# Kernel tuning notes

Measured on AMD Instinct MI355X. Metric: run time of the kernel, lower is better.

The kernel has to match this reference:

```python
import jax, jax.numpy as jnp
import numpy as np

N = 4096          # number of bodies
DIM = 2           # 2D physics (Parallax robot soccer)
K_BROAD = 4 * N   # broad phase keeps first 4N AABB overlaps (per source)
K_EXACT = N       # exact phase keeps first N true penetrations (per source)


def setup_inputs() -> dict:
    key = jax.random.key(0)
    k1, k2 = jax.random.split(key)
    # disk bodies scattered in a ~160x160 arena -> dense enough for many hits
    pos = jax.random.normal(k1, (N, DIM), dtype=jnp.float32) * 40.0
    radius = jax.random.uniform(k2, (N,), dtype=jnp.float32, minval=0.5, maxval=1.5)
    return {"pos": pos, "radius": radius}


def _forward(pos, radius):
    n = pos.shape[0]
    # ---- broad phase: sphere AABB = pos +- radius; two boxes overlap iff
    # |p_i - p_j| <= r_i + r_j on every axis. Full O(N^2) scan (as in source),
    # compact the first K_BROAD hits in row-major (i*n + j) order.
    d = jnp.abs(pos[:, None, :] - pos[None, :, :])            # [N,N,DIM]
    rsum = radius[:, None] + radius[None, :]                  # [N,N]
    overlap = jnp.all(d <= rsum[..., None], axis=-1)          # [N,N] bool
    overlap = overlap & ~jnp.eye(n, dtype=bool)               # skip self-pairs
    flat = overlap.reshape(-1)                                # [N*N]
    rank = jnp.cumsum(flat.astype(jnp.int32)) - 1             # slot of each hit
    valid = flat & (rank < K_BROAD)
    slot = jnp.where(valid, rank, K_BROAD)                    # K_BROAD -> dropped
    ii = jnp.repeat(jnp.arange(n, dtype=jnp.int32), n)
    jj = jnp.tile(jnp.arange(n, dtype=jnp.int32), n)
    bi = jnp.full((K_BROAD,), -1, jnp.int32).at[slot].set(ii, mode='drop')
    bj = jnp.full((K_BROAD,), -1, jnp.int32).at[slot].set(jj, mode='drop')
    # ---- exact phase: sphere-sphere penetration test on broad pairs,
    # keep first K_EXACT real penetrations (gather-compute-compact).
    gi = jnp.clip(bi, 0, n - 1)
    gj = jnp.clip(bj, 0, n - 1)
    dv = pos[gi] - pos[gj]                                    # [K_BROAD,DIM]
    dist = jnp.sqrt(jnp.sum(dv * dv, axis=-1) + 1e-12)
    pen_depth = radius[gi] + radius[gj] - dist                # >0 means overlap
    hit = (bi >= 0) & (pen_depth > 0)
    erank = jnp.cumsum(hit.astype(jnp.int32)) - 1
    evalid = hit & (erank < K_EXACT)
    eslot = jnp.where(evalid, erank, K_EXACT)                 # K_EXACT -> dropped
    pen_vec = dv * (pen_depth / dist)[:, None]                # penetration vector
    ei = jnp.full((K_EXACT,), -1, jnp.int32).at[eslot].set(bi, mode='drop')
    ej = jnp.full((K_EXACT,), -1, jnp.int32).at[eslot].set(bj, mode='drop')
    ev = jnp.zeros((K_EXACT, pos.shape[-1]), pos.dtype).at[eslot].set(pen_vec, mode='drop')
    # ---- resolve: each body of the pair is pushed half the penetration apart,
    si = jnp.where(ei >= 0, ei, n)                            # n -> dropped
    sj = jnp.where(ej >= 0, ej, n)
    new_i = pos[jnp.clip(ei, 0, n - 1)] + 0.5 * ev
    new_j = pos[jnp.clip(ej, 0, n - 1)] - 0.5 * ev
    out = pos.at[si].set(new_i, mode='drop')
    out = out.at[sj].set(new_j, mode='drop')
    return out


def reference(pos, radius):
    return _forward(pos, radius)
```

## Files before the change

### kernel.cpp

```cpp
#include <hip/hip_runtime.h>

#define NB 4096
#define KBROAD (4 * NB)
#define KEXACT NB
typedef unsigned long long u64;

__global__ __launch_bounds__(256) void count_kernel(
    const float2* __restrict__ pos, const float* __restrict__ rad,
    int* __restrict__ row_counts, u64* __restrict__ masks,
    int* __restrict__ last_key) {
  int gid = blockIdx.x * blockDim.x + threadIdx.x;
  if (gid < NB) last_key[gid] = -1;
  int wave = gid >> 6;
  int lane = gid & 63;
  int r0 = wave * 2;
  float2 p0 = pos[r0], p1 = pos[r0 + 1];
  float ra0 = rad[r0], ra1 = rad[r0 + 1];
  u64 mw0 = 0, mw1 = 0;
  int c0 = 0, c1 = 0;
  for (int c = 0; c < 64; ++c) {
    int j = c * 64 + lane;
    float2 pj = pos[j];
    float rj = rad[j];
    float rs0 = ra0 + rj, rs1 = ra1 + rj;
    bool h0 = (j != r0) && (fabsf(p0.x - pj.x) <= rs0) && (fabsf(p0.y - pj.y) <= rs0);
    bool h1 = (j != r0 + 1) && (fabsf(p1.x - pj.x) <= rs1) && (fabsf(p1.y - pj.y) <= rs1);
    u64 m0 = __ballot(h0);
    u64 m1 = __ballot(h1);
    if (lane == c) { mw0 = m0; mw1 = m1; }
    c0 += __popcll(m0);
    c1 += __popcll(m1);
  }
  masks[(size_t)r0 * 64 + lane] = mw0;
  masks[(size_t)(r0 + 1) * 64 + lane] = mw1;
  if (lane == 0) { row_counts[r0] = c0; row_counts[r0 + 1] = c1; }
}

__global__ __launch_bounds__(256) void fill_kernel(
    const float2* __restrict__ pos, const float* __restrict__ rad,
    const int* __restrict__ row_counts, const u64* __restrict__ masks,
    float2* __restrict__ penvec, unsigned* __restrict__ pij,
    int* __restrict__ totalp) {
  __shared__ int rb[NB];
  __shared__ int wsum[4];
  int t = threadIdx.x;
  int wv = t >> 6, lane = t & 63;
  int c[16], s = 0;
  #pragma unroll
  for (int k = 0; k < 16; ++k) { c[k] = row_counts[t * 16 + k]; s += c[k]; }
  int v = s;
  #pragma unroll
  for (int off = 1; off < 64; off <<= 1) {
    int u = __shfl_up(v, off);
    if (lane >= off) v += u;
  }
  if (lane == 63) wsum[wv] = v;
  __syncthreads();
  int wbase = 0;
  #pragma unroll
  for (int w = 0; w < 4; ++w) if (w < wv) wbase += wsum[w];
  int run = wbase + v - s;
  #pragma unroll
  for (int k = 0; k < 16; ++k) { rb[k * 256 + t] = run; run += c[k]; }
  if (blockIdx.x == 0 && t == 255) totalp[0] = run;
  __syncthreads();
  for (int q = 0; q < 4; ++q) {
    int r = blockIdx.x * 16 + wv * 4 + q;
    int rowbase = rb[(r & 15) * 256 + (r >> 4)];
    if (rowbase >= KBROAD) continue;
    u64 myw = masks[(size_t)r * 64 + lane];
    int cnt = __popcll(myw);
    int v2 = cnt;
    #pragma unroll
    for (int off = 1; off < 64; off <<= 1) {
      int u = __shfl_up(v2, off);
      if (lane >= off) v2 += u;
    }
    int rank = rowbase + v2 - cnt;
    if (!myw) continue;
    float2 pr = pos[r];
    float rr = rad[r];
    u64 m = myw;
    while (m && rank < KBROAD) {
      int b = __builtin_ctzll(m);
      m &= m - 1;
      int j = (lane << 6) + b;
      float2 pj = pos[j];
      float dx = pr.x - pj.x, dy = pr.y - pj.y;
      float ss = __fadd_rn(__fadd_rn(__fmul_rn(dx, dx), __fmul_rn(dy, dy)), 1e-12f);
      float dist = __fsqrt_rn(ss);
      float pen = __fsub_rn(__fadd_rn(rr, rad[j]), dist);
      if (pen > 0.0f) {
        float sc = __fdiv_rn(pen, dist);
        penvec[rank] = make_float2(__fmul_rn(dx, sc), __fmul_rn(dy, sc));
        pij[rank] = ((unsigned)r << 16) | (unsigned)j;
      }
      ++rank;
    }
  }
}

__global__ __launch_bounds__(256) void exact_kernel(
    const unsigned* __restrict__ pij, const float2* __restrict__ penvec,
    const int* __restrict__ totalp, float2* __restrict__ ev,
    int* __restrict__ last_key) {
  __shared__ u64 bm[256];
  __shared__ int eb[256];
  __shared__ int wsum[4];
  int t = threadIdx.x;
  int wv = t >> 6, lane = t & 63;
  int total = totalp[0];
  if (total > KBROAD) total = KBROAD;
  u64 m = 0;
  int base = t * 64;
  #pragma unroll
  for (int k = 0; k < 16; ++k) {
    uint4 d = ((const uint4*)pij)[t * 16 + k];
    int s = base + 4 * k;
    unsigned n = 0;
    n |= (((d.x & 0xF000F000u) == 0u) && (s + 0 < total)) ? 1u : 0u;
    n |= (((d.y & 0xF000F000u) == 0u) && (s + 1 < total)) ? 2u : 0u;
    n |= (((d.z & 0xF000F000u) == 0u) && (s + 2 < total)) ? 4u : 0u;
    n |= (((d.w & 0xF000F000u) == 0u) && (s + 3 < total)) ? 8u : 0u;
    m |= (u64)n << (4 * k);
  }
  int cnt = __popcll(m);
  int v = cnt;
  #pragma unroll
  for (int off = 1; off < 64; off <<= 1) {
    int u = __shfl_up(v, off);
    if (lane >= off) v += u;
  }
  if (lane == 63) wsum[wv] = v;
  bm[t] = m;
  __syncthreads();
  int wbase = 0;
  #pragma unroll
  for (int w = 0; w < 4; ++w) if (w < wv) wbase += wsum[w];
  eb[t] = wbase + v - cnt;
  __syncthreads();
  int s = blockIdx.x * 256 + t;
  u64 w = bm[s >> 6];
  if ((w >> (s & 63)) & 1ull) {
    int rank = eb[s >> 6] + __popcll(w & (((u64)1 << (s & 63)) - 1ull));
    if (rank < KEXACT) {
      ev[rank] = penvec[s];
      unsigned p = pij[s];
      atomicMax(&last_key[p >> 16], rank);
      atomicMax(&last_key[p & 0xFFFFu], 0x10000 | rank);
    }
  }
}

__global__ __launch_bounds__(256) void combine_kernel(
    const float2* __restrict__ pos, const int* __restrict__ last_key,
    const float2* __restrict__ ev, float2* __restrict__ out) {
  int b = blockIdx.x * blockDim.x + threadIdx.x;
  float2 p = pos[b];
  int k = last_key[b];
  float2 o = p;
  if (k >= 0) {
    int rank = k & 0xFFFF;
    float2 e = ev[rank];
    if (k & 0x10000) {
      o.x = __fsub_rn(p.x, __fmul_rn(0.5f, e.x));
      o.y = __fsub_rn(p.y, __fmul_rn(0.5f, e.y));
    } else {
      o.x = __fadd_rn(p.x, __fmul_rn(0.5f, e.x));
      o.y = __fadd_rn(p.y, __fmul_rn(0.5f, e.y));
    }
  }
  out[b] = o;
}

extern "C" void kernel_launch(void* const* d_in, const int* in_sizes, int n_in,
                              void* d_out, int out_size, void* d_ws, size_t ws_size,
                              hipStream_t stream) {
  const float2* pos = (const float2*)d_in[0];
  const float* rad = (const float*)d_in[1];
  float2* out = (float2*)d_out;

  unsigned* pij = (unsigned*)d_ws;
  float2* penvec = (float2*)(pij + KBROAD);
  float2* ev = penvec + KBROAD;
  u64* masks = (u64*)(ev + KEXACT);
  int* row_counts = (int*)(masks + (size_t)NB * 64);
  int* totalp = row_counts + NB;
  int* last_key = totalp + 1;

  count_kernel<<<512, 256, 0, stream>>>(pos, rad, row_counts, masks, last_key);
  fill_kernel<<<256, 256, 0, stream>>>(pos, rad, row_counts, masks, penvec,
                                       pij, totalp);
  exact_kernel<<<64, 256, 0, stream>>>(pij, penvec, totalp, ev, last_key);
  combine_kernel<<<16, 256, 0, stream>>>(pos, last_key, ev, out);
}
```

Before: 93.27 us.

## Fuse exact-phase compaction and combine into one kernel with shared-memory last-writer table

Merges the exact-compaction and combine kernels into a single kernel. Each of 16 blocks redundantly recomputes the full exact compaction, writing penetration vectors and last-writer keys into shared memory instead of global buffers. This removes one launch, the global last_key init, and the global atomics and round-trips. The cost is redundant serial per-thread work in every block, plus heavier shared-memory use that includes a 32KB ev array. It also vectorises the row_counts load in the fill kernel as int4.

```diff
diff --git a/kernel.cpp b/kernel.cpp
--- a/kernel.cpp
+++ b/kernel.cpp
@@ -7,10 +7,8 @@
 
 __global__ __launch_bounds__(256) void count_kernel(
     const float2* __restrict__ pos, const float* __restrict__ rad,
-    int* __restrict__ row_counts, u64* __restrict__ masks,
-    int* __restrict__ last_key) {
+    int* __restrict__ row_counts, u64* __restrict__ masks) {
   int gid = blockIdx.x * blockDim.x + threadIdx.x;
-  if (gid < NB) last_key[gid] = -1;
   int wave = gid >> 6;
   int lane = gid & 63;
   int r0 = wave * 2;
@@ -47,7 +45,12 @@
   int wv = t >> 6, lane = t & 63;
   int c[16], s = 0;
   #pragma unroll
-  for (int k = 0; k < 16; ++k) { c[k] = row_counts[t * 16 + k]; s += c[k]; }
+  for (int k4 = 0; k4 < 4; ++k4) {
+    int4 d = ((const int4*)row_counts)[t * 4 + k4];
+    c[4 * k4 + 0] = d.x; c[4 * k4 + 1] = d.y;
+    c[4 * k4 + 2] = d.z; c[4 * k4 + 3] = d.w;
+    s += d.x + d.y + d.z + d.w;
+  }
   int v = s;
   #pragma unroll
   for (int off = 1; off < 64; off <<= 1) {
@@ -100,15 +103,19 @@
   }
 }
 
-__global__ __launch_bounds__(256) void exact_kernel(
-    const unsigned* __restrict__ pij, const float2* __restrict__ penvec,
-    const int* __restrict__ totalp, float2* __restrict__ ev,
-    int* __restrict__ last_key) {
+__global__ __launch_bounds__(256) void final_kernel(
+    const float2* __restrict__ pos, const unsigned* __restrict__ pij,
+    const float2* __restrict__ penvec, const int* __restrict__ totalp,
+    float2* __restrict__ out) {
   __shared__ u64 bm[256];
   __shared__ int eb[256];
   __shared__ int wsum[4];
+  __shared__ int lastk[NB];
+  __shared__ float2 ev[KEXACT];
   int t = threadIdx.x;
   int wv = t >> 6, lane = t & 63;
+  #pragma unroll
+  for (int k = 0; k < 16; ++k) lastk[k * 256 + t] = -1;
   int total = totalp[0];
   if (total > KBROAD) total = KBROAD;
   u64 m = 0;
@@ -138,30 +145,25 @@
   #pragma unroll
   for (int w = 0; w < 4; ++w) if (w < wv) wbase += wsum[w];
   eb[t] = wbase + v - cnt;
+  int rank = eb[t];
+  u64 w = m;
+  while (w && rank < KEXACT) {
+    int bit = __builtin_ctzll(w);
+    w &= w - 1;
+    int s = base + bit;
+    ev[rank] = penvec[s];
+    unsigned p = pij[s];
+    atomicMax(&lastk[p >> 16], rank);
+    atomicMax(&lastk[p & 0xFFFFu], 0x10000 | rank);
+    ++rank;
+  }
   __syncthreads();
-  int s = blockIdx.x * 256 + t;
-  u64 w = bm[s >> 6];
-  if ((w >> (s & 63)) & 1ull) {
-    int rank = eb[s >> 6] + __popcll(w & (((u64)1 << (s & 63)) - 1ull));
-    if (rank < KEXACT) {
-      ev[rank] = penvec[s];
-      unsigned p = pij[s];
-      atomicMax(&last_key[p >> 16], rank);
-      atomicMax(&last_key[p & 0xFFFFu], 0x10000 | rank);
-    }
-  }
-}
-
-__global__ __launch_bounds__(256) void combine_kernel(
-    const float2* __restrict__ pos, const int* __restrict__ last_key,
-    const float2* __restrict__ ev, float2* __restrict__ out) {
-  int b = blockIdx.x * blockDim.x + threadIdx.x;
+  int b = blockIdx.x * 256 + t;
   float2 p = pos[b];
-  int k = last_key[b];
+  int k = lastk[b];
   float2 o = p;
   if (k >= 0) {
-    int rank = k & 0xFFFF;
-    float2 e = ev[rank];
+    float2 e = ev[k & 0xFFFF];
     if (k & 0x10000) {
       o.x = __fsub_rn(p.x, __fmul_rn(0.5f, e.x));
       o.y = __fsub_rn(p.y, __fmul_rn(0.5f, e.y));
@@ -182,15 +184,12 @@
 
   unsigned* pij = (unsigned*)d_ws;
   float2* penvec = (float2*)(pij + KBROAD);
-  float2* ev = penvec + KBROAD;
-  u64* masks = (u64*)(ev + KEXACT);
+  u64* masks = (u64*)(penvec + KBROAD);
   int* row_counts = (int*)(masks + (size_t)NB * 64);
   int* totalp = row_counts + NB;
-  int* last_key = totalp + 1;
 
-  count_kernel<<<512, 256, 0, stream>>>(pos, rad, row_counts, masks, last_key);
+  count_kernel<<<512, 256, 0, stream>>>(pos, rad, row_counts, masks);
   fill_kernel<<<256, 256, 0, stream>>>(pos, rad, row_counts, masks, penvec,
                                        pij, totalp);
-  exact_kernel<<<64, 256, 0, stream>>>(pij, penvec, totalp, ev, last_key);
-  combine_kernel<<<16, 256, 0, stream>>>(pos, last_key, ev, out);
+  final_kernel<<<16, 256, 0, stream>>>(pos, pij, penvec, totalp, out);
 }
```

Measured after the change: 104.4 us. +12.0%, slower.
